# Kernel tuning notes

Measured on AMD Instinct MI355X. Metric: run time of the kernel, lower is better.

Reference implementation:

```python
import jax, jax.numpy as jnp
import numpy as np
import math

B, T, S = 32, 512, 256          # batch, tgt_len (prediction_length), src_len (encoder tokens)
PD, ED = 1, 768                 # pred_dim, encoder_dim
D, H, L, FF = 256, 8, 4, 1024   # d_model, nhead, num_layers, dim_feedforward
HD = D // H
NEG = -1e9
EPS = 1e-5


def _pos_encoding(seq_len, d_model):
    pos = jnp.arange(seq_len, dtype=jnp.float32)[:, None]
    div = jnp.exp(jnp.arange(0, d_model, 2, dtype=jnp.float32) * (-math.log(10000.0) / d_model))
    pe = jnp.zeros((seq_len, d_model), jnp.float32)
    pe = pe.at[:, 0::2].set(jnp.sin(pos * div))
    pe = pe.at[:, 1::2].set(jnp.cos(pos * div))
    return pe


def _ln(x, g, b):
    m = jnp.mean(x, -1, keepdims=True)
    v = jnp.mean((x - m) ** 2, -1, keepdims=True)
    return (x - m) * jax.lax.rsqrt(v + EPS) * g + b


def _mha(xq, xkv, Wq, bq, Wk, bk, Wv, bv, Wo, bo, mask):
    b, t, d = xq.shape
    s = xkv.shape[1]
    Q = (xq @ Wq + bq).reshape(b, t, H, HD).transpose(0, 2, 1, 3)   # bhtd
    K = (xkv @ Wk + bk).reshape(b, s, H, HD).transpose(0, 2, 1, 3)  # bhsd
    V = (xkv @ Wv + bv).reshape(b, s, H, HD).transpose(0, 2, 1, 3)
    scores = jnp.einsum('bhtd,bhsd->bhts', Q, K) * (HD ** -0.5)
    if mask is not None:
        scores = scores + mask
    w = jax.nn.softmax(scores, axis=-1)
    o = jnp.einsum('bhts,bhsd->bhtd', w, V).transpose(0, 2, 1, 3).reshape(b, t, d)
    return o @ Wo + bo


def _forward(tgt, memory, W_emb, b_emb, W_enc, b_enc,
             Wq_s, bq_s, Wk_s, bk_s, Wv_s, bv_s, Wo_s, bo_s,
             Wq_c, bq_c, Wk_c, bk_c, Wv_c, bv_c, Wo_c, bo_c,
             g1, be1, g2, be2, g3, be3, Wf1, bf1, Wf2, bf2,
             Wp1, bp1, Wp2, bp2):
    t = tgt.shape[1]
    x = tgt @ W_emb + b_emb + _pos_encoding(t, D)          # (B,T,D)
    mem = memory @ W_enc + b_enc                           # (B,S,D)
    causal = jnp.triu(jnp.full((t, t), NEG, jnp.float32), k=1)
    for i in range(L):
        sa = _mha(x, x, Wq_s[i], bq_s[i], Wk_s[i], bk_s[i], Wv_s[i], bv_s[i], Wo_s[i], bo_s[i], causal)
        x = _ln(x + sa, g1[i], be1[i])
        ca = _mha(x, mem, Wq_c[i], bq_c[i], Wk_c[i], bk_c[i], Wv_c[i], bv_c[i], Wo_c[i], bo_c[i], None)
        x = _ln(x + ca, g2[i], be2[i])
        ff = jax.nn.gelu(x @ Wf1[i] + bf1[i], approximate=False) @ Wf2[i] + bf2[i]
        x = _ln(x + ff, g3[i], be3[i])
    h = jax.nn.gelu(x @ Wp1 + bp1, approximate=False)
    return h @ Wp2 + bp2                                   # (B,T,PD)


def setup_inputs() -> dict:
    key = jax.random.key(0)
    keys = iter(jax.random.split(key, 40))
    def rn(shape, scale=0.05):
        return jax.random.normal(next(keys), shape, jnp.float32) * scale
    z = jnp.zeros
    inp = {
        'tgt': jax.random.normal(next(keys), (B, T, PD), jnp.float32),
        'memory': jax.random.normal(next(keys), (B, S, ED), jnp.float32),
        'W_emb': rn((PD, D)), 'b_emb': z((D,)),
        'W_enc': rn((ED, D)), 'b_enc': z((D,)),
        'Wq_s': rn((L, D, D)), 'bq_s': z((L, D)),
        'Wk_s': rn((L, D, D)), 'bk_s': z((L, D)),
        'Wv_s': rn((L, D, D)), 'bv_s': z((L, D)),
        'Wo_s': rn((L, D, D)), 'bo_s': z((L, D)),
        'Wq_c': rn((L, D, D)), 'bq_c': z((L, D)),
        'Wk_c': rn((L, D, D)), 'bk_c': z((L, D)),
        'Wv_c': rn((L, D, D)), 'bv_c': z((L, D)),
        'Wo_c': rn((L, D, D)), 'bo_c': z((L, D)),
        'g1': jnp.ones((L, D)), 'be1': z((L, D)),
        'g2': jnp.ones((L, D)), 'be2': z((L, D)),
        'g3': jnp.ones((L, D)), 'be3': z((L, D)),
        'Wf1': rn((L, D, FF)), 'bf1': z((L, FF)),
        'Wf2': rn((L, FF, D)), 'bf2': z((L, D)),
        'Wp1': rn((D, D // 2)), 'bp1': z((D // 2,)),
        'Wp2': rn((D // 2, PD), 0.01), 'bp2': jnp.full((PD,), 0.1, jnp.float32),
    }
    return inp


def reference(tgt, memory, W_emb, b_emb, W_enc, b_enc,
              Wq_s, bq_s, Wk_s, bk_s, Wv_s, bv_s, Wo_s, bo_s,
              Wq_c, bq_c, Wk_c, bk_c, Wv_c, bv_c, Wo_c, bo_c,
              g1, be1, g2, be2, g3, be3, Wf1, bf1, Wf2, bf2,
              Wp1, bp1, Wp2, bp2):
    return _forward(tgt, memory, W_emb, b_emb, W_enc, b_enc,
                    Wq_s, bq_s, Wk_s, bk_s, Wv_s, bv_s, Wo_s, bo_s,
                    Wq_c, bq_c, Wk_c, bk_c, Wv_c, bv_c, Wo_c, bo_c,
                    g1, be1, g2, be2, g3, be3, Wf1, bf1, Wf2, bf2,
                    Wp1, bp1, Wp2, bp2)
```

## Files before the change

kernel.cpp:

```cpp
#include <hip/hip_runtime.h>
#include <math.h>

#define B_  32
#define T_  512
#define S_  256
#define D_  256
#define H_  8
#define HD_ 32
#define FF_ 1024
#define ED_ 768
#define L_  4
#define BT_ (B_*T_)
#define BS_ (B_*S_)

typedef __bf16 bf16x8_t __attribute__((ext_vector_type(8)));
typedef __bf16 bf16x4_t __attribute__((ext_vector_type(4)));
typedef float  f32x4_t  __attribute__((ext_vector_type(4)));

__device__ __forceinline__ float gelu_f(float v) {
  return 0.5f * v * (1.f + erff(v * 0.7071067811865476f));
}

__device__ __forceinline__ void gl16(const __bf16* gsrc, __bf16* ldst) {
  __builtin_amdgcn_global_load_lds(
      (const __attribute__((address_space(1))) unsigned int*)gsrc,
      (__attribute__((address_space(3))) unsigned int*)ldst, 16, 0, 0);
}

__global__ __launch_bounds__(256)
void embed_kernel(const float* __restrict__ tgt, const float* __restrict__ Wemb,
                  const float* __restrict__ bemb, float* __restrict__ x,
                  __bf16* __restrict__ xbf) {
  int i = blockIdx.x * 256 + threadIdx.x;
  int d  = i & (D_ - 1);
  int bt = i >> 8;
  int t  = bt & (T_ - 1);
  int p  = d >> 1;
  float div = expf((float)(2 * p) * (-9.210340371976184f / (float)D_));
  float arg = (float)t * div;
  float pe = (d & 1) ? cosf(arg) : sinf(arg);
  float v = tgt[bt] * Wemb[d] + bemb[d] + pe;
  x[i] = v;
  xbf[i] = (__bf16)v;
}

__global__ __launch_bounds__(256)
void cvt_bf16_kernel(const float* __restrict__ in, __bf16* __restrict__ out) {
  int i = (blockIdx.x * 256 + threadIdx.x) * 4;
  float4 v = *(const float4*)(in + i);
  bf16x4_t o;
  o[0] = (__bf16)v.x; o[1] = (__bf16)v.y; o[2] = (__bf16)v.z; o[3] = (__bf16)v.w;
  *(bf16x4_t*)(out + i) = o;
}

struct TD { const float* src; size_t dst; int K, N, nb; size_t lstride; };
struct TDs { TD d[12]; };

__global__ __launch_bounds__(256)
void transpose_cvt_kernel(TDs a, __bf16* __restrict__ wt) {
  __shared__ float tile[32][33];
  TD t = a.d[blockIdx.y];
  const int kt = t.K >> 5, nt = t.N >> 5;
  const int per = kt * nt, tot = per * t.nb;
  const int id = blockIdx.x;
  if (id >= tot) return;
  const int b = id / per;
  const int r2 = id - b * per;
  const int kti = r2 / nt;
  const int nti = r2 - kti * nt;
  const int c = threadIdx.x & 31, r0 = threadIdx.x >> 5;
  const float* src = t.src + (size_t)b * t.K * t.N;
  __bf16* dst = wt + t.dst + (size_t)b * t.lstride;
#pragma unroll
  for (int j = 0; j < 4; ++j) {
    int rr = r0 + j * 8;
    tile[rr][c] = src[(size_t)(kti * 32 + rr) * t.N + nti * 32 + c];
  }
  __syncthreads();
#pragma unroll
  for (int j = 0; j < 4; ++j) {
    int rr = r0 + j * 8;
    dst[(size_t)(nti * 32 + rr) * t.K + kti * 32 + c] = (__bf16)tile[c][rr];
  }
}

__global__ __launch_bounds__(256)
void bias_concat_kernel(const float* __restrict__ bq_s, const float* __restrict__ bk_s,
                        const float* __restrict__ bv_s, const float* __restrict__ bk_c,
                        const float* __restrict__ bv_c, float* __restrict__ dst) {
  int idx = blockIdx.x * 256 + threadIdx.x;
  if (idx >= 5120) return;
  if (idx < 3072) {
    int l = idx / 768, c = idx - l * 768;
    float v = (c < 256) ? bq_s[l * 256 + c]
            : (c < 512) ? bk_s[l * 256 + c - 256]
                        : bv_s[l * 256 + c - 512];
    dst[idx] = v;
  } else {
    int j = idx - 3072;
    int l = j / 512, c = j - l * 512;
    float v = (c < 256) ? bk_c[l * 256 + c] : bv_c[l * 256 + c - 256];
    dst[idx] = v;
  }
}

template<int ACT, int OBF>
__global__ __launch_bounds__(256, 3)
void gemm_bf(const __bf16* __restrict__ A, const __bf16* __restrict__ Bt,
             const float* __restrict__ bias, void* __restrict__ Cv,
             int N, int K, int nN, int ppx) {
  __shared__ __bf16 As[128 * 64];
  __shared__ __bf16 Bs[64 * 64];
  const int tid = threadIdx.x, lane = tid & 63, wv = tid >> 6;
  const int wm = (wv & 1) * 64, wn = (wv >> 1) * 32;
  const int ln15 = lane & 15, kgrp = lane >> 4;
  const int xcd = blockIdx.x & 7, j = blockIdx.x >> 3;
  const int bm = (xcd * ppx + j / nN) * 128;
  const int bn = (j % nN) * 64;

  const int r8 = lane >> 3;
  const int scol = (lane & 7) ^ r8;
  const __bf16* a_g = A  + (size_t)(bm + wv * 32 + r8) * K + scol * 8;
  const __bf16* b_g = Bt + (size_t)(bn + wv * 16 + r8) * K + scol * 8;
  __bf16* a_l = As + wv * 2048;
  __bf16* b_l = Bs + wv * 1024;

  const int xk0 = kgrp ^ (ln15 & 7);
  const int xk1 = (4 + kgrp) ^ (ln15 & 7);

  f32x4_t acc[4][2];
#pragma unroll
  for (int mi = 0; mi < 4; ++mi)
#pragma unroll
    for (int ni = 0; ni < 2; ++ni) acc[mi][ni] = (f32x4_t){0.f, 0.f, 0.f, 0.f};

  for (int k0 = 0; k0 < K; k0 += 64) {
    gl16(a_g + k0,                a_l);
    gl16(a_g + k0 + (size_t)8*K,  a_l + 512);
    gl16(a_g + k0 + (size_t)16*K, a_l + 1024);
    gl16(a_g + k0 + (size_t)24*K, a_l + 1536);
    gl16(b_g + k0,                b_l);
    gl16(b_g + k0 + (size_t)8*K,  b_l + 512);
    __syncthreads();

#pragma unroll
    for (int kk = 0; kk < 2; ++kk) {
      const int xk = kk ? xk1 : xk0;
      bf16x8_t b0 = *(const bf16x8_t*)(Bs + ((wn + ln15) * 8 + xk) * 8);
      bf16x8_t b1 = *(const bf16x8_t*)(Bs + ((wn + 16 + ln15) * 8 + xk) * 8);
#pragma unroll
      for (int mi = 0; mi < 4; ++mi) {
        bf16x8_t af = *(const bf16x8_t*)(As + ((wm + mi * 16 + ln15) * 8 + xk) * 8);
        acc[mi][0] = __builtin_amdgcn_mfma_f32_16x16x32_bf16(af, b0, acc[mi][0], 0, 0, 0);
        acc[mi][1] = __builtin_amdgcn_mfma_f32_16x16x32_bf16(af, b1, acc[mi][1], 0, 0, 0);
      }
    }
    __syncthreads();
  }

#pragma unroll
  for (int mi = 0; mi < 4; ++mi) {
#pragma unroll
    for (int ni = 0; ni < 2; ++ni) {
      const int ocol = bn + wn + ni * 16 + ln15;
      const float bv = bias[ocol];
      const int orow0 = bm + wm + mi * 16 + kgrp * 4;
#pragma unroll
      for (int r = 0; r < 4; ++r) {
        float o = acc[mi][ni][r] + bv;
        if (ACT == 1) o = gelu_f(o);
        if (OBF) ((__bf16*)Cv)[(size_t)(orow0 + r) * N + ocol] = (__bf16)o;
        else     ((float*)Cv)[(size_t)(orow0 + r) * N + ocol] = o;
      }
    }
  }
}

template<int ACT, int OBF>
__global__ __launch_bounds__(256, 3)
void gemm_bf2(const __bf16* __restrict__ A, const __bf16* __restrict__ Bt,
              const float* __restrict__ bias, void* __restrict__ Cv,
              int N, int K, int nN, int ppx) {
  __shared__ __bf16 As[128 * 64];
  __shared__ __bf16 Bs[128 * 64];
  const int tid = threadIdx.x, lane = tid & 63, wv = tid >> 6;
  const int wm = (wv & 1) * 64, wn = (wv >> 1) * 64;
  const int ln15 = lane & 15, kgrp = lane >> 4;
  const int xcd = blockIdx.x & 7, j = blockIdx.x >> 3;
  const int bm = (xcd * ppx + j / nN) * 128;
  const int bn = (j % nN) * 128;

  const int r8 = lane >> 3;
  const int scol = (lane & 7) ^ r8;
  const __bf16* a_g = A  + (size_t)(bm + wv * 32 + r8) * K + scol * 8;
  const __bf16* b_g = Bt + (size_t)(bn + wv * 32 + r8) * K + scol * 8;
  __bf16* a_l = As + wv * 2048;
  __bf16* b_l = Bs + wv * 2048;

  const int xk0 = kgrp ^ (ln15 & 7);
  const int xk1 = (4 + kgrp) ^ (ln15 & 7);

  f32x4_t acc[4][4];
#pragma unroll
  for (int mi = 0; mi < 4; ++mi)
#pragma unroll
    for (int ni = 0; ni < 4; ++ni) acc[mi][ni] = (f32x4_t){0.f, 0.f, 0.f, 0.f};

  for (int k0 = 0; k0 < K; k0 += 64) {
    gl16(a_g + k0,                a_l);
    gl16(a_g + k0 + (size_t)8*K,  a_l + 512);
    gl16(a_g + k0 + (size_t)16*K, a_l + 1024);
    gl16(a_g + k0 + (size_t)24*K, a_l + 1536);
    gl16(b_g + k0,                b_l);
    gl16(b_g + k0 + (size_t)8*K,  b_l + 512);
    gl16(b_g + k0 + (size_t)16*K, b_l + 1024);
    gl16(b_g + k0 + (size_t)24*K, b_l + 1536);
    __syncthreads();

#pragma unroll
    for (int kk = 0; kk < 2; ++kk) {
      const int xk = kk ? xk1 : xk0;
      bf16x8_t bfr[4];
#pragma unroll
      for (int ni = 0; ni < 4; ++ni)
        bfr[ni] = *(const bf16x8_t*)(Bs + ((wn + ni * 16 + ln15) * 8 + xk) * 8);
#pragma unroll
      for (int mi = 0; mi < 4; ++mi) {
        bf16x8_t af = *(const bf16x8_t*)(As + ((wm + mi * 16 + ln15) * 8 + xk) * 8);
#pragma unroll
        for (int ni = 0; ni < 4; ++ni)
          acc[mi][ni] = __builtin_amdgcn_mfma_f32_16x16x32_bf16(af, bfr[ni], acc[mi][ni], 0, 0, 0);
      }
    }
    __syncthreads();
  }

#pragma unroll
  for (int mi = 0; mi < 4; ++mi) {
#pragma unroll
    for (int ni = 0; ni < 4; ++ni) {
      const int ocol = bn + wn + ni * 16 + ln15;
      const float bv = bias[ocol];
      const int orow0 = bm + wm + mi * 16 + kgrp * 4;
#pragma unroll
      for (int r = 0; r < 4; ++r) {
        float o = acc[mi][ni][r] + bv;
        if (ACT == 1) o = gelu_f(o);
        if (OBF) ((__bf16*)Cv)[(size_t)(orow0 + r) * N + ocol] = (__bf16)o;
        else     ((float*)Cv)[(size_t)(orow0 + r) * N + ocol] = o;
      }
    }
  }
}

template<int NEXT_N, int NACT>
__global__ __launch_bounds__(256, 2)
void gemm_ln_next(const __bf16* __restrict__ A, const __bf16* __restrict__ Bt,
                  const float* __restrict__ bias, const float* __restrict__ g,
                  const float* __restrict__ bta, float* __restrict__ x,
                  __bf16* __restrict__ xbf, int K, int ppx,
                  const __bf16* __restrict__ Wn, const float* __restrict__ bn,
                  __bf16* __restrict__ outn) {
  __shared__ __bf16 As[32 * 64];
  __shared__ __bf16 Bs[256 * 64];
  __shared__ __bf16 An[32 * 256];
  __shared__ float red[32][8];
  const int tid = threadIdx.x, lane = tid & 63, wv = tid >> 6;
  const int wn = wv * 64;
  const int ln15 = lane & 15, kgrp = lane >> 4;
  const int xcd = blockIdx.x & 7, j = blockIdx.x >> 3;
  const int bm = (xcd * ppx + j) * 32;

  const int sr = tid >> 3;
  const int sch = (tid & 7) ^ (sr & 7);
  const __bf16* a_g = A  + (size_t)(bm + sr) * K + sch * 8;
  const __bf16* b_g = Bt + (size_t)sr * K + sch * 8;

  f32x4_t acc[2][4];
#pragma unroll
  for (int mi = 0; mi < 2; ++mi)
#pragma unroll
    for (int ni = 0; ni < 4; ++ni) acc[mi][ni] = (f32x4_t){0.f, 0.f, 0.f, 0.f};

  for (int k0 = 0; k0 < K; k0 += 64) {
    gl16(a_g + k0, As + wv * 512);
#pragma unroll
    for (int jj = 0; jj < 8; ++jj)
      gl16(b_g + k0 + (size_t)(jj * 32) * K, Bs + jj * 2048 + wv * 512);
    __syncthreads();
#pragma unroll
    for (int kk = 0; kk < 2; ++kk) {
      bf16x8_t bfr[4];
#pragma unroll
      for (int ni = 0; ni < 4; ++ni) {
        const int nl = wn + ni * 16 + ln15;
        bfr[ni] = *(const bf16x8_t*)(Bs + (nl * 8 + ((kk * 4 + kgrp) ^ (nl & 7))) * 8);
      }
#pragma unroll
      for (int mi = 0; mi < 2; ++mi) {
        const int rl = mi * 16 + ln15;
        bf16x8_t af = *(const bf16x8_t*)(As + (rl * 8 + ((kk * 4 + kgrp) ^ (rl & 7))) * 8);
#pragma unroll
        for (int ni = 0; ni < 4; ++ni)
          acc[mi][ni] = __builtin_amdgcn_mfma_f32_16x16x32_bf16(af, bfr[ni], acc[mi][ni], 0, 0, 0);
      }
    }
    __syncthreads();
  }

  const int c0 = wn + ln15;
  float bs[4], gg[4], bb[4];
#pragma unroll
  for (int ni = 0; ni < 4; ++ni) {
    bs[ni] = bias[c0 + ni * 16];
    gg[ni] = g[c0 + ni * 16];
    bb[ni] = bta[c0 + ni * 16];
  }
  float v[2][4][4];
#pragma unroll
  for (int mi = 0; mi < 2; ++mi) {
#pragma unroll
    for (int r = 0; r < 4; ++r) {
      const int rl = mi * 16 + kgrp * 4 + r;
      const int row = bm + rl;
      float s = 0.f, q = 0.f;
#pragma unroll
      for (int ni = 0; ni < 4; ++ni) {
        float t = acc[mi][ni][r] + bs[ni] + x[(size_t)row * 256 + c0 + ni * 16];
        v[mi][ni][r] = t; s += t; q += t * t;
      }
      s += __shfl_xor(s, 1); s += __shfl_xor(s, 2);
      s += __shfl_xor(s, 4); s += __shfl_xor(s, 8);
      q += __shfl_xor(q, 1); q += __shfl_xor(q, 2);
      q += __shfl_xor(q, 4); q += __shfl_xor(q, 8);
      if (ln15 == 0) {
        red[rl][wv * 2 + 0] = s;
        red[rl][wv * 2 + 1] = q;
      }
    }
  }
  __syncthreads();
#pragma unroll
  for (int mi = 0; mi < 2; ++mi) {
#pragma unroll
    for (int r = 0; r < 4; ++r) {
      const int rl = mi * 16 + kgrp * 4 + r;
      const int row = bm + rl;
      const float ms = red[rl][0] + red[rl][2] + red[rl][4] + red[rl][6];
      const float mq = red[rl][1] + red[rl][3] + red[rl][5] + red[rl][7];
      const float mean = ms * (1.f / 256.f);
      const float var  = mq * (1.f / 256.f) - mean * mean;
      const float rstd = rsqrtf(fmaxf(var, 0.f) + 1e-5f);
#pragma unroll
      for (int ni = 0; ni < 4; ++ni) {
        const int c = c0 + ni * 16;
        float o = (v[mi][ni][r] - mean) * rstd * gg[ni] + bb[ni];
        x[(size_t)row * 256 + c] = o;
        __bf16 ob = (__bf16)o;
        xbf[(size_t)row * 256 + c] = ob;
        if (NEXT_N > 0)
          An[rl * 256 + (((c >> 3) ^ (rl & 7)) << 3) + (c & 7)] = ob;
      }
    }
  }

  if (NEXT_N > 0) {
    for (int pass = 0; pass < NEXT_N / 256; ++pass) {
      const int n0 = pass * 256;
      f32x4_t a2[2][4];
#pragma unroll
      for (int mi = 0; mi < 2; ++mi)
#pragma unroll
        for (int ni = 0; ni < 4; ++ni) a2[mi][ni] = (f32x4_t){0.f, 0.f, 0.f, 0.f};

      for (int k0 = 0; k0 < 256; k0 += 64) {
        const __bf16* wsrc = Wn + (size_t)(n0 + sr) * 256 + k0 + sch * 8;
#pragma unroll
        for (int jj = 0; jj < 8; ++jj)
          gl16(wsrc + (size_t)(jj * 32) * 256, Bs + jj * 2048 + wv * 512);
        __syncthreads();
#pragma unroll
        for (int kk = 0; kk < 2; ++kk) {
          bf16x8_t bfr[4];
#pragma unroll
          for (int ni = 0; ni < 4; ++ni) {
            const int nl = wn + ni * 16 + ln15;
            bfr[ni] = *(const bf16x8_t*)(Bs + (nl * 8 + ((kk * 4 + kgrp) ^ (nl & 7))) * 8);
          }
#pragma unroll
          for (int mi = 0; mi < 2; ++mi) {
            const int row = mi * 16 + ln15;
            const int ck = (k0 >> 3) + kk * 4 + kgrp;
            bf16x8_t af = *(const bf16x8_t*)(An + row * 256 + ((ck ^ (row & 7)) << 3));
#pragma unroll
            for (int ni = 0; ni < 4; ++ni)
              a2[mi][ni] = __builtin_amdgcn_mfma_f32_16x16x32_bf16(af, bfr[ni], a2[mi][ni], 0, 0, 0);
          }
        }
        __syncthreads();
      }
#pragma unroll
      for (int mi = 0; mi < 2; ++mi) {
#pragma unroll
        for (int ni = 0; ni < 4; ++ni) {
          const int ocol = n0 + wn + ni * 16 + ln15;
          const float b2 = bn[ocol];
          const int orow0 = bm + mi * 16 + kgrp * 4;
#pragma unroll
          for (int r = 0; r < 4; ++r) {
            float o = a2[mi][ni][r] + b2;
            if (NACT == 1) o = gelu_f(o);
            outn[(size_t)(orow0 + r) * NEXT_N + ocol] = (__bf16)o;
          }
        }
      }
    }
  }
}

template<bool CAUSAL>
__global__ __launch_bounds__(256)
void attn_mfma(const __bf16* __restrict__ Q, const __bf16* __restrict__ K,
               const __bf16* __restrict__ V, __bf16* __restrict__ O,
               int KVROWS, int qs, int ks) {
  const int b = blockIdx.x >> 3, h = blockIdx.x & 7;
  const int qt = blockIdx.y;
  const int tid = threadIdx.x, lane = tid & 63, wv = tid >> 6;
  const int ln15 = lane & 15, kgrp = lane >> 4, kgrp8 = kgrp * 8;

  __shared__ __bf16 K_lds[64][36];
  __shared__ __bf16 Vt_lds[32][72];
  __shared__ __bf16 P_lds[4][16][72];

  const int q_glob = qt * 64 + wv * 16 + ln15;
  const bf16x8_t qfrag = *(const bf16x8_t*)(Q + (size_t)(b * T_ + q_glob) * qs + h * HD_ + kgrp8);

  const int s_r = tid >> 2, s_c8 = (tid & 3) * 8;
  const __bf16* Kb = K + (size_t)(b * KVROWS + s_r) * ks + h * HD_ + s_c8;
  const __bf16* Vb = V + (size_t)(b * KVROWS + s_r) * ks + h * HD_ + s_c8;

  f32x4_t o0 = (f32x4_t){0.f,0.f,0.f,0.f}, o1 = (f32x4_t){0.f,0.f,0.f,0.f};
  float m = -3.0e38f, l = 0.f;
  const float SCALE = 0.17677669529663689f;
  const int slim = CAUSAL ? (qt + 1) * 64 : KVROWS;

  for (int s0 = 0; s0 < slim; s0 += 64) {
    *(bf16x8_t*)&K_lds[s_r][s_c8] = *(const bf16x8_t*)(Kb + (size_t)s0 * ks);
    bf16x8_t vv = *(const bf16x8_t*)(Vb + (size_t)s0 * ks);
#pragma unroll
    for (int jj = 0; jj < 8; ++jj) Vt_lds[s_c8 + jj][s_r] = vv[jj];
    __syncthreads();

    f32x4_t sa[4];
#pragma unroll
    for (int c = 0; c < 4; ++c) {
      bf16x8_t kf = *(const bf16x8_t*)&K_lds[c * 16 + ln15][kgrp8];
      sa[c] = __builtin_amdgcn_mfma_f32_16x16x32_bf16(kf, qfrag, (f32x4_t){0.f,0.f,0.f,0.f}, 0, 0, 0);
    }
    float v[16];
#pragma unroll
    for (int c = 0; c < 4; ++c)
#pragma unroll
      for (int r = 0; r < 4; ++r) {
        float s = sa[c][r] * SCALE;
        if (CAUSAL && (s0 + c * 16 + kgrp * 4 + r) > q_glob) s += -1e9f;
        v[c * 4 + r] = s;
      }
    float tmax = v[0];
#pragma unroll
    for (int r = 1; r < 16; ++r) tmax = fmaxf(tmax, v[r]);
    tmax = fmaxf(tmax, __shfl_xor(tmax, 16));
    tmax = fmaxf(tmax, __shfl_xor(tmax, 32));
    float mnew = fmaxf(m, tmax);
    float corr = __expf(m - mnew);

    float lsum = 0.f;
#pragma unroll
    for (int c = 0; c < 4; ++c) {
      bf16x4_t pc;
#pragma unroll
      for (int r = 0; r < 4; ++r) {
        float e = __expf(v[c * 4 + r] - mnew);
        lsum += e;
        pc[r] = (__bf16)e;
      }
      *(bf16x4_t*)&P_lds[wv][ln15][c * 16 + kgrp * 4] = pc;
    }
    lsum += __shfl_xor(lsum, 16);
    lsum += __shfl_xor(lsum, 32);
    l = l * corr + lsum;
    m = mnew;

    const float c0 = __shfl(corr, kgrp * 4 + 0);
    const float c1 = __shfl(corr, kgrp * 4 + 1);
    const float c2 = __shfl(corr, kgrp * 4 + 2);
    const float c3 = __shfl(corr, kgrp * 4 + 3);
    o0[0] *= c0; o0[1] *= c1; o0[2] *= c2; o0[3] *= c3;
    o1[0] *= c0; o1[1] *= c1; o1[2] *= c2; o1[3] *= c3;

    bf16x8_t pLo = *(const bf16x8_t*)&P_lds[wv][ln15][kgrp8];
    bf16x8_t pHi = *(const bf16x8_t*)&P_lds[wv][ln15][32 + kgrp8];
    bf16x8_t v0l = *(const bf16x8_t*)&Vt_lds[ln15][kgrp8];
    bf16x8_t v0h = *(const bf16x8_t*)&Vt_lds[ln15][32 + kgrp8];
    bf16x8_t v1l = *(const bf16x8_t*)&Vt_lds[16 + ln15][kgrp8];
    bf16x8_t v1h = *(const bf16x8_t*)&Vt_lds[16 + ln15][32 + kgrp8];
    o0 = __builtin_amdgcn_mfma_f32_16x16x32_bf16(pLo, v0l, o0, 0, 0, 0);
    o0 = __builtin_amdgcn_mfma_f32_16x16x32_bf16(pHi, v0h, o0, 0, 0, 0);
    o1 = __builtin_amdgcn_mfma_f32_16x16x32_bf16(pLo, v1l, o1, 0, 0, 0);
    o1 = __builtin_amdgcn_mfma_f32_16x16x32_bf16(pHi, v1h, o1, 0, 0, 0);
    __syncthreads();
  }

  const float inv = 1.f / l;
  const float i0 = __shfl(inv, kgrp * 4 + 0);
  const float i1 = __shfl(inv, kgrp * 4 + 1);
  const float i2 = __shfl(inv, kgrp * 4 + 2);
  const float i3 = __shfl(inv, kgrp * 4 + 3);
  __bf16* Op = O + (size_t)(b * T_ + qt * 64 + wv * 16 + kgrp * 4) * D_ + h * HD_;
  Op[0 * D_ + ln15] = (__bf16)(o0[0] * i0);  Op[0 * D_ + 16 + ln15] = (__bf16)(o1[0] * i0);
  Op[1 * D_ + ln15] = (__bf16)(o0[1] * i1);  Op[1 * D_ + 16 + ln15] = (__bf16)(o1[1] * i1);
  Op[2 * D_ + ln15] = (__bf16)(o0[2] * i2);  Op[2 * D_ + 16 + ln15] = (__bf16)(o1[2] * i2);
  Op[3 * D_ + ln15] = (__bf16)(o0[3] * i3);  Op[3 * D_ + 16 + ln15] = (__bf16)(o1[3] * i3);
}

__global__ __launch_bounds__(256)
void head2_kernel(const float* __restrict__ hb, const float* __restrict__ w,
                  const float* __restrict__ bias, float* __restrict__ out) {
  const int row = blockIdx.x * 4 + (threadIdx.x >> 6);
  const int lane = threadIdx.x & 63;
  float a = hb[(size_t)row * 128 + lane] * w[lane]
          + hb[(size_t)row * 128 + 64 + lane] * w[64 + lane];
#pragma unroll
  for (int off = 32; off; off >>= 1) a += __shfl_xor(a, off);
  if (lane == 0) out[row] = a + bias[0];
}

extern "C" void kernel_launch(void* const* d_in, const int* in_sizes, int n_in,
                              void* d_out, int out_size, void* d_ws, size_t ws_size,
                              hipStream_t stream) {
  const float* tgt    = (const float*)d_in[0];
  const float* memory = (const float*)d_in[1];
  const float* W_emb  = (const float*)d_in[2];
  const float* b_emb  = (const float*)d_in[3];
  const float* W_enc  = (const float*)d_in[4];
  const float* b_enc  = (const float*)d_in[5];
  const float* Wq_s = (const float*)d_in[6];  const float* bq_s = (const float*)d_in[7];
  const float* Wk_s = (const float*)d_in[8];  const float* bk_s = (const float*)d_in[9];
  const float* Wv_s = (const float*)d_in[10]; const float* bv_s = (const float*)d_in[11];
  const float* Wo_s = (const float*)d_in[12]; const float* bo_s = (const float*)d_in[13];
  const float* Wq_c = (const float*)d_in[14]; const float* bq_c = (const float*)d_in[15];
  const float* Wk_c = (const float*)d_in[16]; const float* bk_c = (const float*)d_in[17];
  const float* Wv_c = (const float*)d_in[18]; const float* bv_c = (const float*)d_in[19];
  const float* Wo_c = (const float*)d_in[20]; const float* bo_c = (const float*)d_in[21];
  const float* g1  = (const float*)d_in[22]; const float* be1 = (const float*)d_in[23];
  const float* g2  = (const float*)d_in[24]; const float* be2 = (const float*)d_in[25];
  const float* g3  = (const float*)d_in[26]; const float* be3 = (const float*)d_in[27];
  const float* Wf1 = (const float*)d_in[28]; const float* bf1 = (const float*)d_in[29];
  const float* Wf2 = (const float*)d_in[30]; const float* bf2 = (const float*)d_in[31];
  const float* Wp1 = (const float*)d_in[32]; const float* bp1 = (const float*)d_in[33];
  const float* Wp2 = (const float*)d_in[34]; const float* bp2 = (const float*)d_in[35];

  float*  x     = (float*)d_ws;
  __bf16* xbf   = (__bf16*)(x + (size_t)4194304);
  __bf16* membf = xbf + (size_t)4194304;
  __bf16* wt    = (__bf16*)((float*)membf + 1048576);
  float*  bcat  = (float*)(wt + 4423680);
  __bf16* kvall = (__bf16*)(bcat + 8192);
  __bf16* qkv   = kvall + (size_t)16777216;
  __bf16* ff    = qkv + (size_t)12582912;
  __bf16* qc    = ff + (size_t)16777216;
  __bf16* ao    = qc + (size_t)4194304;
  __bf16* memb = ff;
  float*  hbuf = (float*)qc;

  const size_t o_enc  = 0;
  const size_t o_qkv  = 196608;
  const size_t o_qcw  = 983040;
  const size_t o_kvw  = 1245184;
  const size_t o_os   = 1769472;
  const size_t o_oc   = 2031616;
  const size_t o_f1   = 2293760;
  const size_t o_f2   = 3342336;
  const size_t o_p1   = 4390912;

  TDs td;
  td.d[0]  = {W_enc, o_enc,           ED_, D_,  1, 0};
  td.d[1]  = {Wq_s,  o_qkv + 0,       D_,  D_,  L_, 196608};
  td.d[2]  = {Wk_s,  o_qkv + 65536,   D_,  D_,  L_, 196608};
  td.d[3]  = {Wv_s,  o_qkv + 131072,  D_,  D_,  L_, 196608};
  td.d[4]  = {Wq_c,  o_qcw,           D_,  D_,  L_, 65536};
  td.d[5]  = {Wk_c,  o_kvw + 0,       D_,  D_,  L_, 131072};
  td.d[6]  = {Wv_c,  o_kvw + 65536,   D_,  D_,  L_, 131072};
  td.d[7]  = {Wo_s,  o_os,            D_,  D_,  L_, 65536};
  td.d[8]  = {Wo_c,  o_oc,            D_,  D_,  L_, 65536};
  td.d[9]  = {Wf1,   o_f1,            D_,  FF_, L_, 262144};
  td.d[10] = {Wf2,   o_f2,            FF_, D_,  L_, 262144};
  td.d[11] = {Wp1,   o_p1,            D_,  128, 1, 0};

  dim3 blk(256);
  cvt_bf16_kernel<<<BS_ * ED_ / 1024, blk, 0, stream>>>(memory, memb);
  transpose_cvt_kernel<<<dim3(1024, 12), blk, 0, stream>>>(td, wt);
  bias_concat_kernel<<<20, blk, 0, stream>>>(bq_s, bk_s, bv_s, bk_c, bv_c, bcat);
  embed_kernel<<<BT_ * D_ / 256, blk, 0, stream>>>(tgt, W_emb, b_emb, x, xbf);

  const float* bqkv = bcat;
  const float* bkv  = bcat + 3072;
  const dim3 gA(B_ * H_, T_ / 64);

  gemm_bf<0,1><<<64 * 4, blk, 0, stream>>>(memb, wt + o_enc, b_enc, membf, D_, ED_, 4, 8);
  gemm_bf2<0,1><<<64 * 16, blk, 0, stream>>>(membf, wt + o_kvw, bkv, kvall, 2048, D_, 16, 8);
  gemm_bf2<0,1><<<128 * 6, blk, 0, stream>>>(xbf, wt + o_qkv, bqkv, qkv, 768, D_, 6, 16);

  for (int i = 0; i < L_; ++i) {
    attn_mfma<true><<<gA, blk, 0, stream>>>(qkv, qkv + 256, qkv + 512, ao, T_, 768, 768);
    gemm_ln_next<256,0><<<512, blk, 0, stream>>>(
        ao, wt + o_os + (size_t)i * 65536, bo_s + i * D_, g1 + i * D_, be1 + i * D_,
        x, xbf, D_, 64, wt + o_qcw + (size_t)i * 65536, bq_c + i * D_, qc);
    attn_mfma<false><<<gA, blk, 0, stream>>>(qc, kvall + i * 512, kvall + i * 512 + 256, ao, S_, 256, 2048);
    gemm_ln_next<1024,1><<<512, blk, 0, stream>>>(
        ao, wt + o_oc + (size_t)i * 65536, bo_c + i * D_, g2 + i * D_, be2 + i * D_,
        x, xbf, D_, 64, wt + o_f1 + (size_t)i * 262144, bf1 + i * FF_, ff);
    if (i < L_ - 1) {
      gemm_ln_next<768,0><<<512, blk, 0, stream>>>(
          ff, wt + o_f2 + (size_t)i * 262144, bf2 + i * D_, g3 + i * D_, be3 + i * D_,
          x, xbf, FF_, 64, wt + o_qkv + (size_t)(i + 1) * 196608, bqkv + (i + 1) * 768, qkv);
    } else {
      gemm_ln_next<0,0><<<512, blk, 0, stream>>>(
          ff, wt + o_f2 + (size_t)i * 262144, bf2 + i * D_, g3 + i * D_, be3 + i * D_,
          x, xbf, FF_, 64, (const __bf16*)nullptr, (const float*)nullptr, (__bf16*)nullptr);
    }
  }
  gemm_bf<1,0><<<128 * 2, blk, 0, stream>>>(xbf, wt + o_p1, bp1, hbuf, 128, D_, 2, 16);
  head2_kernel<<<BT_ / 4, blk, 0, stream>>>(hbuf, Wp2, bp2, (float*)d_out);
}
```

Before: 684.1 us.

## Load GEMM operands directly from global memory instead of LDS staging in gemm_ln_next

After: 961.1 us. 1.4x slower.

```diff
diff --git a/kernel.cpp b/kernel.cpp
--- a/kernel.cpp
+++ b/kernel.cpp
@@ -261,8 +261,6 @@
                   __bf16* __restrict__ xbf, int K, int ppx,
                   const __bf16* __restrict__ Wn, const float* __restrict__ bn,
                   __bf16* __restrict__ outn) {
-  __shared__ __bf16 As[32 * 64];
-  __shared__ __bf16 Bs[256 * 64];
   __shared__ __bf16 An[32 * 256];
   __shared__ float red[32][8];
   const int tid = threadIdx.x, lane = tid & 63, wv = tid >> 6;
@@ -271,41 +269,38 @@
   const int xcd = blockIdx.x & 7, j = blockIdx.x >> 3;
   const int bm = (xcd * ppx + j) * 32;
 
-  const int sr = tid >> 3;
-  const int sch = (tid & 7) ^ (sr & 7);
-  const __bf16* a_g = A  + (size_t)(bm + sr) * K + sch * 8;
-  const __bf16* b_g = Bt + (size_t)sr * K + sch * 8;
-
   f32x4_t acc[2][4];
 #pragma unroll
   for (int mi = 0; mi < 2; ++mi)
 #pragma unroll
     for (int ni = 0; ni < 4; ++ni) acc[mi][ni] = (f32x4_t){0.f, 0.f, 0.f, 0.f};
 
-  for (int k0 = 0; k0 < K; k0 += 64) {
-    gl16(a_g + k0, As + wv * 512);
-#pragma unroll
-    for (int jj = 0; jj < 8; ++jj)
-      gl16(b_g + k0 + (size_t)(jj * 32) * K, Bs + jj * 2048 + wv * 512);
-    __syncthreads();
-#pragma unroll
-    for (int kk = 0; kk < 2; ++kk) {
-      bf16x8_t bfr[4];
-#pragma unroll
-      for (int ni = 0; ni < 4; ++ni) {
-        const int nl = wn + ni * 16 + ln15;
-        bfr[ni] = *(const bf16x8_t*)(Bs + (nl * 8 + ((kk * 4 + kgrp) ^ (nl & 7))) * 8);
-      }
-#pragma unroll
-      for (int mi = 0; mi < 2; ++mi) {
-        const int rl = mi * 16 + ln15;
-        bf16x8_t af = *(const bf16x8_t*)(As + (rl * 8 + ((kk * 4 + kgrp) ^ (rl & 7))) * 8);
-#pragma unroll
-        for (int ni = 0; ni < 4; ++ni)
-          acc[mi][ni] = __builtin_amdgcn_mfma_f32_16x16x32_bf16(af, bfr[ni], acc[mi][ni], 0, 0, 0);
-      }
-    }
-    __syncthreads();
+  {
+    const __bf16* a0p = A + (size_t)(bm + ln15) * K;
+    const __bf16* a1p = A + (size_t)(bm + 16 + ln15) * K;
+    const __bf16* b0p = Bt + (size_t)(wn + ln15) * K;
+    const __bf16* b1p = Bt + (size_t)(wn + 16 + ln15) * K;
+    const __bf16* b2p = Bt + (size_t)(wn + 32 + ln15) * K;
+    const __bf16* b3p = Bt + (size_t)(wn + 48 + ln15) * K;
+    const int kb0 = kgrp * 8;
+#pragma unroll 4
+    for (int ks = 0; ks < K / 32; ++ks) {
+      const int kb = kb0 + ks * 32;
+      bf16x8_t af0 = *(const bf16x8_t*)(a0p + kb);
+      bf16x8_t af1 = *(const bf16x8_t*)(a1p + kb);
+      bf16x8_t bf0 = *(const bf16x8_t*)(b0p + kb);
+      bf16x8_t bf1 = *(const bf16x8_t*)(b1p + kb);
+      bf16x8_t bf2 = *(const bf16x8_t*)(b2p + kb);
+      bf16x8_t bf3 = *(const bf16x8_t*)(b3p + kb);
+      acc[0][0] = __builtin_amdgcn_mfma_f32_16x16x32_bf16(af0, bf0, acc[0][0], 0, 0, 0);
+      acc[1][0] = __builtin_amdgcn_mfma_f32_16x16x32_bf16(af1, bf0, acc[1][0], 0, 0, 0);
+      acc[0][1] = __builtin_amdgcn_mfma_f32_16x16x32_bf16(af0, bf1, acc[0][1], 0, 0, 0);
+      acc[1][1] = __builtin_amdgcn_mfma_f32_16x16x32_bf16(af1, bf1, acc[1][1], 0, 0, 0);
+      acc[0][2] = __builtin_amdgcn_mfma_f32_16x16x32_bf16(af0, bf2, acc[0][2], 0, 0, 0);
+      acc[1][2] = __builtin_amdgcn_mfma_f32_16x16x32_bf16(af1, bf2, acc[1][2], 0, 0, 0);
+      acc[0][3] = __builtin_amdgcn_mfma_f32_16x16x32_bf16(af0, bf3, acc[0][3], 0, 0, 0);
+      acc[1][3] = __builtin_amdgcn_mfma_f32_16x16x32_bf16(af1, bf3, acc[1][3], 0, 0, 0);
+    }
   }
 
   const int c0 = wn + ln15;
@@ -365,39 +360,39 @@
   }
 
   if (NEXT_N > 0) {
+    __syncthreads();
+    const int kb0 = kgrp * 8;
+#pragma unroll
     for (int pass = 0; pass < NEXT_N / 256; ++pass) {
       const int n0 = pass * 256;
+      const __bf16* w0p = Wn + (size_t)(n0 + wn + ln15) * 256;
+      const __bf16* w1p = Wn + (size_t)(n0 + wn + 16 + ln15) * 256;
+      const __bf16* w2p = Wn + (size_t)(n0 + wn + 32 + ln15) * 256;
+      const __bf16* w3p = Wn + (size_t)(n0 + wn + 48 + ln15) * 256;
       f32x4_t a2[2][4];
 #pragma unroll
       for (int mi = 0; mi < 2; ++mi)
 #pragma unroll
         for (int ni = 0; ni < 4; ++ni) a2[mi][ni] = (f32x4_t){0.f, 0.f, 0.f, 0.f};
-
-      for (int k0 = 0; k0 < 256; k0 += 64) {
-        const __bf16* wsrc = Wn + (size_t)(n0 + sr) * 256 + k0 + sch * 8;
-#pragma unroll
-        for (int jj = 0; jj < 8; ++jj)
-          gl16(wsrc + (size_t)(jj * 32) * 256, Bs + jj * 2048 + wv * 512);
-        __syncthreads();
-#pragma unroll
-        for (int kk = 0; kk < 2; ++kk) {
-          bf16x8_t bfr[4];
-#pragma unroll
-          for (int ni = 0; ni < 4; ++ni) {
-            const int nl = wn + ni * 16 + ln15;
-            bfr[ni] = *(const bf16x8_t*)(Bs + (nl * 8 + ((kk * 4 + kgrp) ^ (nl & 7))) * 8);
-          }
-#pragma unroll
-          for (int mi = 0; mi < 2; ++mi) {
-            const int row = mi * 16 + ln15;
-            const int ck = (k0 >> 3) + kk * 4 + kgrp;
-            bf16x8_t af = *(const bf16x8_t*)(An + row * 256 + ((ck ^ (row & 7)) << 3));
-#pragma unroll
-            for (int ni = 0; ni < 4; ++ni)
-              a2[mi][ni] = __builtin_amdgcn_mfma_f32_16x16x32_bf16(af, bfr[ni], a2[mi][ni], 0, 0, 0);
-          }
-        }
-        __syncthreads();
+#pragma unroll
+      for (int ks = 0; ks < 8; ++ks) {
+        const int kb = kb0 + ks * 32;
+        const int ck = ks * 4 + kgrp;
+        const int r0l = ln15, r1l = 16 + ln15;
+        bf16x8_t af0 = *(const bf16x8_t*)(An + r0l * 256 + ((ck ^ (r0l & 7)) << 3));
+        bf16x8_t af1 = *(const bf16x8_t*)(An + r1l * 256 + ((ck ^ (r1l & 7)) << 3));
+        bf16x8_t bf0 = *(const bf16x8_t*)(w0p + kb);
+        bf16x8_t bf1 = *(const bf16x8_t*)(w1p + kb);
+        bf16x8_t bf2 = *(const bf16x8_t*)(w2p + kb);
+        bf16x8_t bf3 = *(const bf16x8_t*)(w3p + kb);
+        a2[0][0] = __builtin_amdgcn_mfma_f32_16x16x32_bf16(af0, bf0, a2[0][0], 0, 0, 0);
+        a2[1][0] = __builtin_amdgcn_mfma_f32_16x16x32_bf16(af1, bf0, a2[1][0], 0, 0, 0);
+        a2[0][1] = __builtin_amdgcn_mfma_f32_16x16x32_bf16(af0, bf1, a2[0][1], 0, 0, 0);
+        a2[1][1] = __builtin_amdgcn_mfma_f32_16x16x32_bf16(af1, bf1, a2[1][1], 0, 0, 0);
+        a2[0][2] = __builtin_amdgcn_mfma_f32_16x16x32_bf16(af0, bf2, a2[0][2], 0, 0, 0);
+        a2[1][2] = __builtin_amdgcn_mfma_f32_16x16x32_bf16(af1, bf2, a2[1][2], 0, 0, 0);
+        a2[0][3] = __builtin_amdgcn_mfma_f32_16x16x32_bf16(af0, bf3, a2[0][3], 0, 0, 0);
+        a2[1][3] = __builtin_amdgcn_mfma_f32_16x16x32_bf16(af1, bf3, a2[1][3], 0, 0, 0);
       }
 #pragma unroll
       for (int mi = 0; mi < 2; ++mi) {
```

## Split fused LN+next-GEMM across two blocks per row tile, ping-pong residual buffers

Applied to the files above, without the earlier changes.

New measurement: 781.9 us. +14.3%, slower.

```diff
diff --git a/kernel.cpp b/kernel.cpp
--- a/kernel.cpp
+++ b/kernel.cpp
@@ -253,12 +253,13 @@
   }
 }
 
-template<int NEXT_N, int NACT>
+template<int NEXT_N, int NACT, int NSPLIT, int WXBF>
 __global__ __launch_bounds__(256, 2)
 void gemm_ln_next(const __bf16* __restrict__ A, const __bf16* __restrict__ Bt,
                   const float* __restrict__ bias, const float* __restrict__ g,
-                  const float* __restrict__ bta, float* __restrict__ x,
-                  __bf16* __restrict__ xbf, int K, int ppx,
+                  const float* __restrict__ bta, const float* __restrict__ xin,
+                  float* __restrict__ xout, __bf16* __restrict__ xbf,
+                  int K, int ppx,
                   const __bf16* __restrict__ Wn, const float* __restrict__ bn,
                   __bf16* __restrict__ outn) {
   __shared__ __bf16 As[32 * 64];
@@ -268,7 +269,9 @@
   const int tid = threadIdx.x, lane = tid & 63, wv = tid >> 6;
   const int wn = wv * 64;
   const int ln15 = lane & 15, kgrp = lane >> 4;
-  const int xcd = blockIdx.x & 7, j = blockIdx.x >> 3;
+  const int sp = (NSPLIT > 1) ? (blockIdx.x >> 9) : 0;
+  const int b2 = blockIdx.x & 511;
+  const int xcd = b2 & 7, j = b2 >> 3;
   const int bm = (xcd * ppx + j) * 32;
 
   const int sr = tid >> 3;
@@ -326,7 +329,7 @@
       float s = 0.f, q = 0.f;
 #pragma unroll
       for (int ni = 0; ni < 4; ++ni) {
-        float t = acc[mi][ni][r] + bs[ni] + x[(size_t)row * 256 + c0 + ni * 16];
+        float t = acc[mi][ni][r] + bs[ni] + xin[(size_t)row * 256 + c0 + ni * 16];
         v[mi][ni][r] = t; s += t; q += t * t;
       }
       s += __shfl_xor(s, 1); s += __shfl_xor(s, 2);
@@ -355,9 +358,11 @@
       for (int ni = 0; ni < 4; ++ni) {
         const int c = c0 + ni * 16;
         float o = (v[mi][ni][r] - mean) * rstd * gg[ni] + bb[ni];
-        x[(size_t)row * 256 + c] = o;
         __bf16 ob = (__bf16)o;
-        xbf[(size_t)row * 256 + c] = ob;
+        if (sp == 0) {
+          xout[(size_t)row * 256 + c] = o;
+          if (WXBF) xbf[(size_t)row * 256 + c] = ob;
+        }
         if (NEXT_N > 0)
           An[rl * 256 + (((c >> 3) ^ (rl & 7)) << 3) + (c & 7)] = ob;
       }
@@ -365,7 +370,7 @@
   }
 
   if (NEXT_N > 0) {
-    for (int pass = 0; pass < NEXT_N / 256; ++pass) {
+    for (int pass = sp; pass < NEXT_N / 256; pass += NSPLIT) {
       const int n0 = pass * 256;
       f32x4_t a2[2][4];
 #pragma unroll
@@ -404,11 +409,11 @@
 #pragma unroll
         for (int ni = 0; ni < 4; ++ni) {
           const int ocol = n0 + wn + ni * 16 + ln15;
-          const float b2 = bn[ocol];
+          const float b2v = bn[ocol];
           const int orow0 = bm + mi * 16 + kgrp * 4;
 #pragma unroll
           for (int r = 0; r < 4; ++r) {
-            float o = a2[mi][ni][r] + b2;
+            float o = a2[mi][ni][r] + b2v;
             if (NACT == 1) o = gelu_f(o);
             outn[(size_t)(orow0 + r) * NEXT_N + ocol] = (__bf16)o;
           }
@@ -560,8 +565,8 @@
   const float* Wp1 = (const float*)d_in[32]; const float* bp1 = (const float*)d_in[33];
   const float* Wp2 = (const float*)d_in[34]; const float* bp2 = (const float*)d_in[35];
 
-  float*  x     = (float*)d_ws;
-  __bf16* xbf   = (__bf16*)(x + (size_t)4194304);
+  float*  x0    = (float*)d_ws;
+  __bf16* xbf   = (__bf16*)(x0 + (size_t)4194304);
   __bf16* membf = xbf + (size_t)4194304;
   __bf16* wt    = (__bf16*)((float*)membf + 1048576);
   float*  bcat  = (float*)(wt + 4423680);
@@ -570,6 +575,7 @@
   __bf16* ff    = qkv + (size_t)12582912;
   __bf16* qc    = ff + (size_t)16777216;
   __bf16* ao    = qc + (size_t)4194304;
+  float*  x1    = (float*)(ao + (size_t)4194304);
   __bf16* memb = ff;
   float*  hbuf = (float*)qc;
 
@@ -601,7 +607,7 @@
   cvt_bf16_kernel<<<BS_ * ED_ / 1024, blk, 0, stream>>>(memory, memb);
   transpose_cvt_kernel<<<dim3(1024, 12), blk, 0, stream>>>(td, wt);
   bias_concat_kernel<<<20, blk, 0, stream>>>(bq_s, bk_s, bv_s, bk_c, bv_c, bcat);
-  embed_kernel<<<BT_ * D_ / 256, blk, 0, stream>>>(tgt, W_emb, b_emb, x, xbf);
+  embed_kernel<<<BT_ * D_ / 256, blk, 0, stream>>>(tgt, W_emb, b_emb, x0, xbf);
 
   const float* bqkv = bcat;
   const float* bkv  = bcat + 3072;
@@ -611,24 +617,29 @@
   gemm_bf2<0,1><<<64 * 16, blk, 0, stream>>>(membf, wt + o_kvw, bkv, kvall, 2048, D_, 16, 8);
   gemm_bf2<0,1><<<128 * 6, blk, 0, stream>>>(xbf, wt + o_qkv, bqkv, qkv, 768, D_, 6, 16);
 
+  float* xin = x0;
+  float* xout = x1;
   for (int i = 0; i < L_; ++i) {
     attn_mfma<true><<<gA, blk, 0, stream>>>(qkv, qkv + 256, qkv + 512, ao, T_, 768, 768);
-    gemm_ln_next<256,0><<<512, blk, 0, stream>>>(
+    gemm_ln_next<256,0,1,0><<<512, blk, 0, stream>>>(
         ao, wt + o_os + (size_t)i * 65536, bo_s + i * D_, g1 + i * D_, be1 + i * D_,
-        x, xbf, D_, 64, wt + o_qcw + (size_t)i * 65536, bq_c + i * D_, qc);
+        xin, xout, xbf, D_, 64, wt + o_qcw + (size_t)i * 65536, bq_c + i * D_, qc);
+    { float* t = xin; xin = xout; xout = t; }
     attn_mfma<false><<<gA, blk, 0, stream>>>(qc, kvall + i * 512, kvall + i * 512 + 256, ao, S_, 256, 2048);
-    gemm_ln_next<1024,1><<<512, blk, 0, stream>>>(
+    gemm_ln_next<1024,1,2,0><<<1024, blk, 0, stream>>>(
         ao, wt + o_oc + (size_t)i * 65536, bo_c + i * D_, g2 + i * D_, be2 + i * D_,
-        x, xbf, D_, 64, wt + o_f1 + (size_t)i * 262144, bf1 + i * FF_, ff);
+        xin, xout, xbf, D_, 64, wt + o_f1 + (size_t)i * 262144, bf1 + i * FF_, ff);
+    { float* t = xin; xin = xout; xout = t; }
     if (i < L_ - 1) {
-      gemm_ln_next<768,0><<<512, blk, 0, stream>>>(
+      gemm_ln_next<768,0,2,0><<<1024, blk, 0, stream>>>(
           ff, wt + o_f2 + (size_t)i * 262144, bf2 + i * D_, g3 + i * D_, be3 + i * D_,
-          x, xbf, FF_, 64, wt + o_qkv + (size_t)(i + 1) * 196608, bqkv + (i + 1) * 768, qkv);
+          xin, xout, xbf, FF_, 64, wt + o_qkv + (size_t)(i + 1) * 196608, bqkv + (i + 1) * 768, qkv);
     } else {
-      gemm_ln_next<0,0><<<512, blk, 0, stream>>>(
+      gemm_ln_next<0,0,1,1><<<512, blk, 0, stream>>>(
           ff, wt + o_f2 + (size_t)i * 262144, bf2 + i * D_, g3 + i * D_, be3 + i * D_,
-          x, xbf, FF_, 64, (const __bf16*)nullptr, (const float*)nullptr, (__bf16*)nullptr);
-    }
+          xin, xout, xbf, FF_, 64, (const __bf16*)nullptr, (const float*)nullptr, (__bf16*)nullptr);
+    }
+    { float* t = xin; xin = xout; xout = t; }
   }
   gemm_bf<1,0><<<128 * 2, blk, 0, stream>>>(xbf, wt + o_p1, bp1, hbuf, 128, D_, 2, 16);
   head2_kernel<<<BT_ / 4, blk, 0, stream>>>(hbuf, Wp2, bp2, (float*)d_out);
```
